# Optimization experiments

Hardware: AMD Instinct MI355X
Metric: run time of the kernel (lower is better)

## Reference

```python
import jax, jax.numpy as jnp
import numpy as np

I, H, NL = 153, 128, 2


def setup_inputs() -> dict:
    key = jax.random.key(0)
    ks = jax.random.split(key, 16)
    s = 1.0 / np.sqrt(H)
    inp = {"x": jax.random.normal(ks[0], (1024, 256, I), dtype=jnp.float32)}
    # GRU layer 0 (input I) and layer 1 (input H), PyTorch layout: W_ih [3H, in], W_hh [3H, H]
    inp["W_ih0"] = jax.random.uniform(ks[1], (3 * H, I), jnp.float32, -s, s)
    inp["W_hh0"] = jax.random.uniform(ks[2], (3 * H, H), jnp.float32, -s, s)
    inp["b_ih0"] = jax.random.uniform(ks[3], (3 * H,), jnp.float32, -s, s)
    inp["b_hh0"] = jax.random.uniform(ks[4], (3 * H,), jnp.float32, -s, s)
    inp["W_ih1"] = jax.random.uniform(ks[5], (3 * H, H), jnp.float32, -s, s)
    inp["W_hh1"] = jax.random.uniform(ks[6], (3 * H, H), jnp.float32, -s, s)
    inp["b_ih1"] = jax.random.uniform(ks[7], (3 * H,), jnp.float32, -s, s)
    inp["b_hh1"] = jax.random.uniform(ks[8], (3 * H,), jnp.float32, -s, s)
    # head: Linear(H,64) -> ReLU -> Linear(64,1) -> Sigmoid (dropout = eval no-op)
    s1 = 1.0 / np.sqrt(H)
    s2 = 1.0 / np.sqrt(64)
    inp["W1"] = jax.random.uniform(ks[9], (64, H), jnp.float32, -s1, s1)
    inp["b1"] = jax.random.uniform(ks[10], (64,), jnp.float32, -s1, s1)
    inp["W2"] = jax.random.uniform(ks[11], (1, 64), jnp.float32, -s2, s2)
    inp["b2"] = jax.random.uniform(ks[12], (1,), jnp.float32, -s2, s2)
    return inp


def _gru_layer(x, W_ih, W_hh, b_ih, b_hh, return_seq):
    # x: [B, T, in]; PyTorch GRU cell equations.
    B, T, _ = x.shape
    gi = jnp.einsum('bti,gi->btg', x, W_ih) + b_ih  # [B, T, 3H] input projection (one big GEMM)
    gi = jnp.transpose(gi, (1, 0, 2))  # [T, B, 3H]
    h0 = jnp.zeros((B, H), dtype=x.dtype)

    def step(h, gi_t):
        gh = h @ W_hh.T + b_hh  # [B, 3H]
        i_r, i_z, i_n = jnp.split(gi_t, 3, axis=-1)
        h_r, h_z, h_n = jnp.split(gh, 3, axis=-1)
        r = jax.nn.sigmoid(i_r + h_r)
        z = jax.nn.sigmoid(i_z + h_z)
        n = jnp.tanh(i_n + r * h_n)
        h_new = (1.0 - z) * n + z * h
        return h_new, (h_new if return_seq else 0.0)

    h_last, ys = jax.lax.scan(step, h0, gi)
    if return_seq:
        return jnp.transpose(ys, (1, 0, 2))  # [B, T, H]
    return h_last  # [B, H]


def reference(x, W_ih0, W_hh0, b_ih0, b_hh0, W_ih1, W_hh1, b_ih1, b_hh1, W1, b1, W2, b2):
    seq0 = _gru_layer(x, W_ih0, W_hh0, b_ih0, b_hh0, return_seq=True)
    last = _gru_layer(seq0, W_ih1, W_hh1, b_ih1, b_hh1, return_seq=False)  # out[:, -1, :]
    hdn = jax.nn.relu(last @ W1.T + b1)
    return jax.nn.sigmoid(hdn @ W2.T + b2)  # [B, 1]
```

## Files before the change

### kernel.cpp

```cpp
#include <hip/hip_runtime.h>


typedef __bf16 bf16x8 __attribute__((ext_vector_type(8)));
typedef __bf16 bf16x4 __attribute__((ext_vector_type(4)));
typedef float  f32x4  __attribute__((ext_vector_type(4)));

#define HS 136
#define OS 136
#define AS 168

__device__ __forceinline__ f32x4 mfma16(bf16x8 a, bf16x8 b, f32x4 c) {
    return __builtin_amdgcn_mfma_f32_16x16x32_bf16(a, b, c, 0, 0, 0);
}
__device__ __forceinline__ float sigf(float x) {
    return __builtin_amdgcn_rcpf(1.f + __expf(-x));
}
__device__ __forceinline__ float tanhf_(float x) { return 2.f * sigf(2.f * x) - 1.f; }

__device__ __forceinline__ void barrier_nodrain() {
    asm volatile("s_waitcnt lgkmcnt(0)" ::: "memory");
    __builtin_amdgcn_s_barrier();
    asm volatile("" ::: "memory");
}

__global__ void prep_w_kernel(const float* __restrict__ Wih0, const float* __restrict__ Whh0,
                              const float* __restrict__ Wih1, const float* __restrict__ Whh1,
                              __bf16* __restrict__ o_ih0, __bf16* __restrict__ o_hh0,
                              __bf16* __restrict__ o_ih1, __bf16* __restrict__ o_hh1) {
    int idx = blockIdx.x * 256 + threadIdx.x;
    if (idx < 384 * 160) {
        int n = idx / 160, k = idx - n * 160;
        o_ih0[idx] = (__bf16)(k < 153 ? Wih0[n * 153 + k] : 0.f);
    }
    if (idx < 384 * 128) {
        o_hh0[idx] = (__bf16)Whh0[idx];
        o_ih1[idx] = (__bf16)Wih1[idx];
        o_hh1[idx] = (__bf16)Whh1[idx];
    }
}

__global__ __launch_bounds__(512, 2) void gi0_gemm_kernel(
    const float* __restrict__ x, const __bf16* __restrict__ Wih0b,
    __bf16* __restrict__ gi0)
{
    __shared__ __align__(16) __bf16 smem[128 * AS];
    const int r0  = blockIdx.x * 128;
    const int tid = threadIdx.x;
    const int w = tid >> 6, lane = tid & 63, q = lane >> 4, c15 = lane & 15;

    bf16x8 bf[3][5];
    #pragma unroll
    for (int j = 0; j < 3; ++j) {
        int colb = 16 * (w + 8 * j) + c15;
        #pragma unroll
        for (int ks = 0; ks < 5; ++ks)
            bf[j][ks] = *(const bf16x8*)(Wih0b + colb * 160 + ks * 32 + q * 8);
    }

    const float* px = x + (size_t)r0 * 153;
    auto scatter = [&](unsigned c, f32x4 v) {
        unsigned m0  = 4u * c;
        unsigned row = m0 / 153u;
        unsigned col = m0 - row * 153u;
        #pragma unroll
        for (int i = 0; i < 4; ++i) {
            unsigned cc = col + i, rr = row;
            if (cc >= 153u) { cc -= 153u; rr += 1u; }
            smem[rr * AS + cc] = (__bf16)v[i];
        }
    };
    #pragma unroll
    for (int p = tid; p < 896; p += 512)
        smem[(p / 7) * AS + 153 + p % 7] = (__bf16)0.f;
    {
        f32x4 v[5];
        #pragma unroll
        for (int k = 0; k < 5; ++k)
            v[k] = *(const f32x4*)(px + 4u * (tid + k * 512));
        #pragma unroll
        for (int k = 0; k < 5; ++k) scatter(tid + k * 512, v[k]);
        f32x4 u[4];
        #pragma unroll
        for (int k = 0; k < 4; ++k)
            u[k] = *(const f32x4*)(px + 4u * (tid + (5 + k) * 512));
        f32x4 tv;
        const bool tail = tid < 288;
        if (tail) tv = *(const f32x4*)(px + 4u * (tid + 4608));
        #pragma unroll
        for (int k = 0; k < 4; ++k) scatter(tid + (5 + k) * 512, u[k]);
        if (tail) scatter(tid + 4608, tv);
    }
    barrier_nodrain();

    f32x4 acc[8][3];
    #pragma unroll
    for (int rt = 0; rt < 8; ++rt)
        #pragma unroll
        for (int j = 0; j < 3; ++j) acc[rt][j] = (f32x4){0.f, 0.f, 0.f, 0.f};

    #pragma unroll
    for (int ks = 0; ks < 5; ++ks) {
        bf16x8 a[8];
        #pragma unroll
        for (int rt = 0; rt < 8; ++rt)
            a[rt] = *(const bf16x8*)(&smem[(rt * 16 + c15) * AS + ks * 32 + q * 8]);
        #pragma unroll
        for (int rt = 0; rt < 8; ++rt)
            #pragma unroll
            for (int j = 0; j < 3; ++j) acc[rt][j] = mfma16(a[rt], bf[j][ks], acc[rt][j]);
    }
    barrier_nodrain();
    #pragma unroll
    for (int j = 0; j < 3; ++j) {
        #pragma unroll
        for (int rt = 0; rt < 8; ++rt)
            #pragma unroll
            for (int r = 0; r < 4; ++r)
                smem[(rt * 16 + q * 4 + r) * OS + 16 * w + c15] = (__bf16)acc[rt][j][r];
        barrier_nodrain();
        #pragma unroll
        for (int pass = 0; pass < 4; ++pass) {
            int row = pass * 32 + (tid >> 4);
            int col = (tid & 15) * 8;
            bf16x8 v = *(const bf16x8*)(&smem[row * OS + col]);
            *(bf16x8*)(gi0 + (size_t)(r0 + row) * 384 + j * 128 + col) = v;
        }
        if (j < 2) barrier_nodrain();
    }
}

__global__ __launch_bounds__(512, 2)
void gru_rec0_kernel(__bf16* __restrict__ gio,
                     const __bf16* __restrict__ Whh0,
                     const float* __restrict__ b_ih0, const float* __restrict__ b_hh0)
{
    __shared__ __align__(16) __bf16 hsA[16 * HS], hsB[16 * HS];

    const int tid  = threadIdx.x;
    const int w    = tid >> 6;
    const int lane = tid & 63;
    const int q    = lane >> 4;
    const int c15  = lane & 15;
    const int c_col = w * 16 + c15;
    const int b0   = blockIdx.x * 16;

    bf16x8 fhh[3][4];
    #pragma unroll
    for (int g = 0; g < 3; ++g)
        #pragma unroll
        for (int ks = 0; ks < 4; ++ks)
            fhh[g][ks] = *(const bf16x8*)(Whh0 + (size_t)(g * 128 + c_col) * 128 + ks * 32 + q * 8);

    float Brz[2], bin, bhn;
    Brz[0] = b_ih0[c_col] + b_hh0[c_col];
    Brz[1] = b_ih0[128 + c_col] + b_hh0[128 + c_col];
    bin = b_ih0[256 + c_col]; bhn = b_hh0[256 + c_col];

    float hr[4] = {0.f, 0.f, 0.f, 0.f};
    for (int i = tid; i < 16 * HS; i += 512) { hsA[i] = (__bf16)0.f; hsB[i] = (__bf16)0.f; }
    __syncthreads();

    unsigned goff[4];
    #pragma unroll
    for (int r = 0; r < 4; ++r)
        goff[r] = (unsigned)(b0 + q * 4 + r) * 98304u + (unsigned)c_col;

    __bf16 gvA[4][3], gvB[4][3];
    #pragma unroll
    for (int r = 0; r < 4; ++r)
        #pragma unroll
        for (int g = 0; g < 3; ++g) gvA[r][g] = gio[goff[r] + g * 128];
    #pragma unroll
    for (int r = 0; r < 4; ++r) goff[r] += 384;

    const int srow = tid >> 5;
    const int scol = (tid & 31) * 4;
    const size_t sbase = (size_t)(b0 + srow) * 98304u + scol;

    auto step = [&](const __bf16* rd, __bf16* wr,
                    __bf16 (&gR)[4][3], __bf16 (&gW)[4][3], int t) {
        #pragma unroll
        for (int r = 0; r < 4; ++r)
            #pragma unroll
            for (int g = 0; g < 3; ++g) gW[r][g] = gio[goff[r] + g * 128];
        #pragma unroll
        for (int r = 0; r < 4; ++r) goff[r] += 384;

        f32x4 hacc[3];
        #pragma unroll
        for (int g = 0; g < 3; ++g) hacc[g] = (f32x4){0.f, 0.f, 0.f, 0.f};
        #pragma unroll
        for (int ks = 0; ks < 4; ++ks) {
            bf16x8 a = *(const bf16x8*)(rd + c15 * HS + ks * 32 + q * 8);
            #pragma unroll
            for (int g = 0; g < 3; ++g) hacc[g] = mfma16(a, fhh[g][ks], hacc[g]);
        }
        #pragma unroll
        for (int r = 0; r < 4; ++r) {
            float rr = sigf((float)gR[r][0] + hacc[0][r] + Brz[0]);
            float zz = sigf((float)gR[r][1] + hacc[1][r] + Brz[1]);
            float nn = tanhf_((float)gR[r][2] + bin + rr * (hacc[2][r] + bhn));
            float hnew = zz * (hr[r] - nn) + nn;
            hr[r] = hnew;
            wr[(q * 4 + r) * HS + c_col] = (__bf16)hnew;
        }
        barrier_nodrain();
        bf16x4 hv = *(const bf16x4*)(wr + srow * HS + scol);
        *(bf16x4*)(gio + sbase + (size_t)t * 384) = hv;
    };

    for (int tt = 0; tt < 128; ++tt) {
        step(hsA, hsB, gvA, gvB, 2 * tt);
        step(hsB, hsA, gvB, gvA, 2 * tt + 1);
    }
}

__global__ __launch_bounds__(512, 2)
void gi1_gemm_kernel(__bf16* __restrict__ gio, const __bf16* __restrict__ Wih1b)
{
    __shared__ __align__(16) __bf16 smem[128 * HS];
    const int r0  = blockIdx.x * 128;
    const int tid = threadIdx.x;
    const int w = tid >> 6, lane = tid & 63, q = lane >> 4, c15 = lane & 15;

    bf16x8 bf[3][4];
    #pragma unroll
    for (int j = 0; j < 3; ++j) {
        int colb = 16 * (w + 8 * j) + c15;
        #pragma unroll
        for (int ks = 0; ks < 4; ++ks)
            bf[j][ks] = *(const bf16x8*)(Wih1b + (size_t)colb * 128 + ks * 32 + q * 8);
    }

    {
        bf16x8 av[4];
        #pragma unroll
        for (int k = 0; k < 4; ++k) {
            int cidx = tid + k * 512;
            int row = cidx >> 4, c8 = (cidx & 15) * 8;
            av[k] = *(const bf16x8*)(gio + (size_t)(r0 + row) * 384 + c8);
        }
        #pragma unroll
        for (int k = 0; k < 4; ++k) {
            int cidx = tid + k * 512;
            int row = cidx >> 4, c8 = (cidx & 15) * 8;
            *(bf16x8*)&smem[row * HS + c8] = av[k];
        }
    }
    barrier_nodrain();

    f32x4 acc[8][3];
    #pragma unroll
    for (int rt = 0; rt < 8; ++rt)
        #pragma unroll
        for (int j = 0; j < 3; ++j) acc[rt][j] = (f32x4){0.f, 0.f, 0.f, 0.f};

    #pragma unroll
    for (int ks = 0; ks < 4; ++ks) {
        bf16x8 a[8];
        #pragma unroll
        for (int rt = 0; rt < 8; ++rt)
            a[rt] = *(const bf16x8*)(&smem[(rt * 16 + c15) * HS + ks * 32 + q * 8]);
        #pragma unroll
        for (int rt = 0; rt < 8; ++rt)
            #pragma unroll
            for (int j = 0; j < 3; ++j) acc[rt][j] = mfma16(a[rt], bf[j][ks], acc[rt][j]);
    }
    barrier_nodrain();
    #pragma unroll
    for (int j = 0; j < 3; ++j) {
        #pragma unroll
        for (int rt = 0; rt < 8; ++rt)
            #pragma unroll
            for (int r = 0; r < 4; ++r)
                smem[(rt * 16 + q * 4 + r) * OS + 16 * w + c15] = (__bf16)acc[rt][j][r];
        barrier_nodrain();
        #pragma unroll
        for (int pass = 0; pass < 4; ++pass) {
            int row = pass * 32 + (tid >> 4);
            int col = (tid & 15) * 8;
            bf16x8 v = *(const bf16x8*)(&smem[row * OS + col]);
            *(bf16x8*)(gio + (size_t)(r0 + row) * 384 + j * 128 + col) = v;
        }
        if (j < 2) barrier_nodrain();
    }
}

__global__ __launch_bounds__(512, 2)
void gru_rec1_kernel(const __bf16* __restrict__ gi1,
                     const __bf16* __restrict__ Whh1,
                     const float* __restrict__ b_ih1, const float* __restrict__ b_hh1,
                     const float* __restrict__ W1, const float* __restrict__ b1,
                     const float* __restrict__ W2, const float* __restrict__ b2,
                     float* __restrict__ out)
{
    __shared__ __align__(16) __bf16 hsA[16 * HS], hsB[16 * HS];
    __shared__ float h1f[16 * 128];
    __shared__ float hdnf[16 * 64];

    const int tid  = threadIdx.x;
    const int w    = tid >> 6;
    const int lane = tid & 63;
    const int q    = lane >> 4;
    const int c15  = lane & 15;
    const int c_col = w * 16 + c15;
    const int b0   = blockIdx.x * 16;

    bf16x8 fhh[3][4];
    #pragma unroll
    for (int g = 0; g < 3; ++g)
        #pragma unroll
        for (int ks = 0; ks < 4; ++ks)
            fhh[g][ks] = *(const bf16x8*)(Whh1 + (size_t)(g * 128 + c_col) * 128 + ks * 32 + q * 8);

    float Brz[2], bin, bhn;
    Brz[0] = b_ih1[c_col] + b_hh1[c_col];
    Brz[1] = b_ih1[128 + c_col] + b_hh1[128 + c_col];
    bin = b_ih1[256 + c_col]; bhn = b_hh1[256 + c_col];

    float hr[4] = {0.f, 0.f, 0.f, 0.f};
    for (int i = tid; i < 16 * HS; i += 512) { hsA[i] = (__bf16)0.f; hsB[i] = (__bf16)0.f; }
    __syncthreads();

    unsigned goff[4];
    #pragma unroll
    for (int r = 0; r < 4; ++r)
        goff[r] = (unsigned)(b0 + q * 4 + r) * 98304u + (unsigned)c_col;

    __bf16 gvA[4][3], gvB[4][3];
    #pragma unroll
    for (int r = 0; r < 4; ++r)
        #pragma unroll
        for (int g = 0; g < 3; ++g) gvA[r][g] = gi1[goff[r] + g * 128];
    #pragma unroll
    for (int r = 0; r < 4; ++r) goff[r] += 384;

    auto step = [&](const __bf16* rd, __bf16* wr,
                    __bf16 (&gR)[4][3], __bf16 (&gW)[4][3]) {
        #pragma unroll
        for (int r = 0; r < 4; ++r)
            #pragma unroll
            for (int g = 0; g < 3; ++g) gW[r][g] = gi1[goff[r] + g * 128];
        #pragma unroll
        for (int r = 0; r < 4; ++r) goff[r] += 384;

        f32x4 hacc[3];
        #pragma unroll
        for (int g = 0; g < 3; ++g) hacc[g] = (f32x4){0.f, 0.f, 0.f, 0.f};
        #pragma unroll
        for (int ks = 0; ks < 4; ++ks) {
            bf16x8 a = *(const bf16x8*)(rd + c15 * HS + ks * 32 + q * 8);
            #pragma unroll
            for (int g = 0; g < 3; ++g) hacc[g] = mfma16(a, fhh[g][ks], hacc[g]);
        }
        #pragma unroll
        for (int r = 0; r < 4; ++r) {
            float rr = sigf((float)gR[r][0] + hacc[0][r] + Brz[0]);
            float zz = sigf((float)gR[r][1] + hacc[1][r] + Brz[1]);
            float nn = tanhf_((float)gR[r][2] + bin + rr * (hacc[2][r] + bhn));
            float hnew = zz * (hr[r] - nn) + nn;
            hr[r] = hnew;
            wr[(q * 4 + r) * HS + c_col] = (__bf16)hnew;
        }
        barrier_nodrain();
    };

    for (int tt = 0; tt < 128; ++tt) {
        step(hsA, hsB, gvA, gvB);
        step(hsB, hsA, gvB, gvA);
    }

    #pragma unroll
    for (int r = 0; r < 4; ++r) h1f[(q * 4 + r) * 128 + c_col] = hr[r];
    __syncthreads();
    for (int p = tid; p < 16 * 64; p += 512) {
        int m = p >> 6, u = p & 63;
        float s = b1[u];
        const float* hrow = &h1f[m * 128];
        const float* wrow = &W1[u * 128];
        #pragma unroll 8
        for (int k = 0; k < 128; ++k) s += hrow[k] * wrow[k];
        hdnf[p] = fmaxf(s, 0.f);
    }
    __syncthreads();
    if (tid < 16) {
        float s = b2[0];
        #pragma unroll 8
        for (int k = 0; k < 64; ++k) s += hdnf[tid * 64 + k] * W2[k];
        out[b0 + tid] = sigf(s);
    }
}

extern "C" void kernel_launch(void* const* d_in, const int* in_sizes, int n_in,
                              void* d_out, int out_size, void* d_ws, size_t ws_size,
                              hipStream_t stream) {
    const float* x     = (const float*)d_in[0];
    const float* W_ih0 = (const float*)d_in[1];
    const float* W_hh0 = (const float*)d_in[2];
    const float* bih0  = (const float*)d_in[3];
    const float* bhh0  = (const float*)d_in[4];
    const float* W_ih1 = (const float*)d_in[5];
    const float* W_hh1 = (const float*)d_in[6];
    const float* bih1  = (const float*)d_in[7];
    const float* bhh1  = (const float*)d_in[8];
    const float* W1    = (const float*)d_in[9];
    const float* b1    = (const float*)d_in[10];
    const float* W2    = (const float*)d_in[11];
    const float* b2    = (const float*)d_in[12];
    float* out = (float*)d_out;

    char* ws = (char*)d_ws;
    __bf16* gio   = (__bf16*)(ws);
    __bf16* wih0b = (__bf16*)(ws + 201326592);
    __bf16* whh0b = (__bf16*)(ws + 201449472);
    __bf16* wih1b = (__bf16*)(ws + 201547776);
    __bf16* whh1b = (__bf16*)(ws + 201646080);

    prep_w_kernel<<<240, 256, 0, stream>>>(W_ih0, W_hh0, W_ih1, W_hh1,
                                           wih0b, whh0b, wih1b, whh1b);
    gi0_gemm_kernel<<<2048, 512, 0, stream>>>(x, wih0b, gio);
    gru_rec0_kernel<<<64, 512, 0, stream>>>(gio, whh0b, bih0, bhh0);
    gi1_gemm_kernel<<<2048, 512, 0, stream>>>(gio, wih1b);
    gru_rec1_kernel<<<64, 512, 0, stream>>>(gio, whh1b, bih1, bhh1,
                                            W1, b1, W2, b2, out);
}
```

Measured before the change: 783.6 us.

## Fuse layer-1 input projection into layer-0 recurrence and store gates time-major

```diff
diff --git a/kernel.cpp b/kernel.cpp
--- a/kernel.cpp
+++ b/kernel.cpp
@@ -2,7 +2,6 @@
 
 
 typedef __bf16 bf16x8 __attribute__((ext_vector_type(8)));
-typedef __bf16 bf16x4 __attribute__((ext_vector_type(4)));
 typedef float  f32x4  __attribute__((ext_vector_type(4)));
 
 #define HS 136
@@ -11,6 +10,10 @@
 
 __device__ __forceinline__ f32x4 mfma16(bf16x8 a, bf16x8 b, f32x4 c) {
     return __builtin_amdgcn_mfma_f32_16x16x32_bf16(a, b, c, 0, 0, 0);
+}
+__device__ __forceinline__ void mfma16_agpr(f32x4& acc, bf16x8 a, const bf16x8& b) {
+    asm("v_mfma_f32_16x16x32_bf16 %0, %1, %2, %0"
+        : "+v"(acc) : "v"(a), "a"(b));
 }
 __device__ __forceinline__ float sigf(float x) {
     return __builtin_amdgcn_rcpf(1.f + __expf(-x));
@@ -47,6 +50,8 @@
     const int r0  = blockIdx.x * 128;
     const int tid = threadIdx.x;
     const int w = tid >> 6, lane = tid & 63, q = lane >> 4, c15 = lane & 15;
+    const int bb = r0 >> 8;
+    const int t0 = r0 & 255;
 
     bf16x8 bf[3][5];
     #pragma unroll
@@ -123,7 +128,8 @@
             int row = pass * 32 + (tid >> 4);
             int col = (tid & 15) * 8;
             bf16x8 v = *(const bf16x8*)(&smem[row * OS + col]);
-            *(bf16x8*)(gi0 + (size_t)(r0 + row) * 384 + j * 128 + col) = v;
+            size_t nrow = (size_t)(t0 + row) * 1024 + bb;
+            *(bf16x8*)(gi0 + nrow * 384 + j * 128 + col) = v;
         }
         if (j < 2) barrier_nodrain();
     }
@@ -132,6 +138,7 @@
 __global__ __launch_bounds__(512, 2)
 void gru_rec0_kernel(__bf16* __restrict__ gio,
                      const __bf16* __restrict__ Whh0,
+                     const __bf16* __restrict__ Wih1b,
                      const float* __restrict__ b_ih0, const float* __restrict__ b_hh0)
 {
     __shared__ __align__(16) __bf16 hsA[16 * HS], hsB[16 * HS];
@@ -144,12 +151,22 @@
     const int c_col = w * 16 + c15;
     const int b0   = blockIdx.x * 16;
 
-    bf16x8 fhh[3][4];
+    bf16x8 fhh[3][4], fih[3][4];
     #pragma unroll
     for (int g = 0; g < 3; ++g)
         #pragma unroll
-        for (int ks = 0; ks < 4; ++ks)
-            fhh[g][ks] = *(const bf16x8*)(Whh0 + (size_t)(g * 128 + c_col) * 128 + ks * 32 + q * 8);
+        for (int ks = 0; ks < 4; ++ks) {
+            size_t off = (size_t)(g * 128 + c_col) * 128 + ks * 32 + q * 8;
+            fhh[g][ks] = *(const bf16x8*)(Whh0 + off);
+            fih[g][ks] = *(const bf16x8*)(Wih1b + off);
+        }
+    #pragma unroll
+    for (int g = 0; g < 3; ++g)
+        #pragma unroll
+        for (int ks = 0; ks < 4; ++ks) {
+            asm volatile("" : "+a"(fhh[g][ks]));
+            asm volatile("" : "+a"(fih[g][ks]));
+        }
 
     float Brz[2], bin, bhn;
     Brz[0] = b_ih0[c_col] + b_hh0[c_col];
@@ -160,40 +177,52 @@
     for (int i = tid; i < 16 * HS; i += 512) { hsA[i] = (__bf16)0.f; hsB[i] = (__bf16)0.f; }
     __syncthreads();
 
-    unsigned goff[4];
+    const size_t TSTRIDE = (size_t)1024 * 384;
+    const __bf16* gp = gio + (size_t)(b0 + q * 4) * 384 + c_col;
+    __bf16*       wp = gio + (size_t)(b0 + q * 4) * 384 + c_col;
+
+    __bf16 gvA[4][3], gvB[4][3];
     #pragma unroll
     for (int r = 0; r < 4; ++r)
-        goff[r] = (unsigned)(b0 + q * 4 + r) * 98304u + (unsigned)c_col;
-
-    __bf16 gvA[4][3], gvB[4][3];
-    #pragma unroll
-    for (int r = 0; r < 4; ++r)
-        #pragma unroll
-        for (int g = 0; g < 3; ++g) gvA[r][g] = gio[goff[r] + g * 128];
-    #pragma unroll
-    for (int r = 0; r < 4; ++r) goff[r] += 384;
-
-    const int srow = tid >> 5;
-    const int scol = (tid & 31) * 4;
-    const size_t sbase = (size_t)(b0 + srow) * 98304u + scol;
-
-    auto step = [&](const __bf16* rd, __bf16* wr,
-                    __bf16 (&gR)[4][3], __bf16 (&gW)[4][3], int t) {
-        #pragma unroll
-        for (int r = 0; r < 4; ++r)
-            #pragma unroll
-            for (int g = 0; g < 3; ++g) gW[r][g] = gio[goff[r] + g * 128];
-        #pragma unroll
-        for (int r = 0; r < 4; ++r) goff[r] += 384;
-
+        #pragma unroll
+        for (int g = 0; g < 3; ++g) gvA[r][g] = gp[r * 384 + g * 128];
+    gp += TSTRIDE;
+
+    auto body = [&](const __bf16* rd, __bf16* wr,
+                    __bf16 (&gR)[4][3], __bf16 (&gW)[4][3],
+                    bool pf, bool st) {
+        if (pf) {
+            #pragma unroll
+            for (int r = 0; r < 4; ++r)
+                #pragma unroll
+                for (int g = 0; g < 3; ++g) gW[r][g] = gp[r * 384 + g * 128];
+            gp += TSTRIDE;
+        }
+        bf16x8 a[4];
+        #pragma unroll
+        for (int ks = 0; ks < 4; ++ks)
+            a[ks] = *(const bf16x8*)(rd + c15 * HS + ks * 32 + q * 8);
         f32x4 hacc[3];
         #pragma unroll
         for (int g = 0; g < 3; ++g) hacc[g] = (f32x4){0.f, 0.f, 0.f, 0.f};
         #pragma unroll
-        for (int ks = 0; ks < 4; ++ks) {
-            bf16x8 a = *(const bf16x8*)(rd + c15 * HS + ks * 32 + q * 8);
-            #pragma unroll
-            for (int g = 0; g < 3; ++g) hacc[g] = mfma16(a, fhh[g][ks], hacc[g]);
+        for (int ks = 0; ks < 4; ++ks)
+            #pragma unroll
+            for (int g = 0; g < 3; ++g) mfma16_agpr(hacc[g], a[ks], fhh[g][ks]);
+        if (st) {
+            f32x4 iacc[3];
+            #pragma unroll
+            for (int g = 0; g < 3; ++g) iacc[g] = (f32x4){0.f, 0.f, 0.f, 0.f};
+            #pragma unroll
+            for (int ks = 0; ks < 4; ++ks)
+                #pragma unroll
+                for (int g = 0; g < 3; ++g) mfma16_agpr(iacc[g], a[ks], fih[g][ks]);
+            #pragma unroll
+            for (int g = 0; g < 3; ++g)
+                #pragma unroll
+                for (int r = 0; r < 4; ++r)
+                    wp[r * 384 + g * 128] = (__bf16)iacc[g][r];
+            wp += TSTRIDE;
         }
         #pragma unroll
         for (int r = 0; r < 4; ++r) {
@@ -205,84 +234,31 @@
             wr[(q * 4 + r) * HS + c_col] = (__bf16)hnew;
         }
         barrier_nodrain();
-        bf16x4 hv = *(const bf16x4*)(wr + srow * HS + scol);
-        *(bf16x4*)(gio + sbase + (size_t)t * 384) = hv;
     };
 
-    for (int tt = 0; tt < 128; ++tt) {
-        step(hsA, hsB, gvA, gvB, 2 * tt);
-        step(hsB, hsA, gvB, gvA, 2 * tt + 1);
-    }
-}
-
-__global__ __launch_bounds__(512, 2)
-void gi1_gemm_kernel(__bf16* __restrict__ gio, const __bf16* __restrict__ Wih1b)
-{
-    __shared__ __align__(16) __bf16 smem[128 * HS];
-    const int r0  = blockIdx.x * 128;
-    const int tid = threadIdx.x;
-    const int w = tid >> 6, lane = tid & 63, q = lane >> 4, c15 = lane & 15;
-
-    bf16x8 bf[3][4];
-    #pragma unroll
-    for (int j = 0; j < 3; ++j) {
-        int colb = 16 * (w + 8 * j) + c15;
-        #pragma unroll
-        for (int ks = 0; ks < 4; ++ks)
-            bf[j][ks] = *(const bf16x8*)(Wih1b + (size_t)colb * 128 + ks * 32 + q * 8);
-    }
-
+    body(hsA, hsB, gvA, gvB, true, false);
+    for (int i = 0; i < 127; ++i) {
+        body(hsB, hsA, gvB, gvA, true, true);
+        body(hsA, hsB, gvA, gvB, true, true);
+    }
+    body(hsB, hsA, gvB, gvA, false, true);
     {
-        bf16x8 av[4];
-        #pragma unroll
-        for (int k = 0; k < 4; ++k) {
-            int cidx = tid + k * 512;
-            int row = cidx >> 4, c8 = (cidx & 15) * 8;
-            av[k] = *(const bf16x8*)(gio + (size_t)(r0 + row) * 384 + c8);
-        }
-        #pragma unroll
-        for (int k = 0; k < 4; ++k) {
-            int cidx = tid + k * 512;
-            int row = cidx >> 4, c8 = (cidx & 15) * 8;
-            *(bf16x8*)&smem[row * HS + c8] = av[k];
-        }
-    }
-    barrier_nodrain();
-
-    f32x4 acc[8][3];
-    #pragma unroll
-    for (int rt = 0; rt < 8; ++rt)
-        #pragma unroll
-        for (int j = 0; j < 3; ++j) acc[rt][j] = (f32x4){0.f, 0.f, 0.f, 0.f};
-
-    #pragma unroll
-    for (int ks = 0; ks < 4; ++ks) {
-        bf16x8 a[8];
-        #pragma unroll
-        for (int rt = 0; rt < 8; ++rt)
-            a[rt] = *(const bf16x8*)(&smem[(rt * 16 + c15) * HS + ks * 32 + q * 8]);
-        #pragma unroll
-        for (int rt = 0; rt < 8; ++rt)
-            #pragma unroll
-            for (int j = 0; j < 3; ++j) acc[rt][j] = mfma16(a[rt], bf[j][ks], acc[rt][j]);
-    }
-    barrier_nodrain();
-    #pragma unroll
-    for (int j = 0; j < 3; ++j) {
-        #pragma unroll
-        for (int rt = 0; rt < 8; ++rt)
+        bf16x8 a[4];
+        #pragma unroll
+        for (int ks = 0; ks < 4; ++ks)
+            a[ks] = *(const bf16x8*)(hsA + c15 * HS + ks * 32 + q * 8);
+        f32x4 iacc[3];
+        #pragma unroll
+        for (int g = 0; g < 3; ++g) iacc[g] = (f32x4){0.f, 0.f, 0.f, 0.f};
+        #pragma unroll
+        for (int ks = 0; ks < 4; ++ks)
+            #pragma unroll
+            for (int g = 0; g < 3; ++g) mfma16_agpr(iacc[g], a[ks], fih[g][ks]);
+        #pragma unroll
+        for (int g = 0; g < 3; ++g)
             #pragma unroll
             for (int r = 0; r < 4; ++r)
-                smem[(rt * 16 + q * 4 + r) * OS + 16 * w + c15] = (__bf16)acc[rt][j][r];
-        barrier_nodrain();
-        #pragma unroll
-        for (int pass = 0; pass < 4; ++pass) {
-            int row = pass * 32 + (tid >> 4);
-            int col = (tid & 15) * 8;
-            bf16x8 v = *(const bf16x8*)(&smem[row * OS + col]);
-            *(bf16x8*)(gio + (size_t)(r0 + row) * 384 + j * 128 + col) = v;
-        }
-        if (j < 2) barrier_nodrain();
+                wp[r * 384 + g * 128] = (__bf16)iacc[g][r];
     }
 }
 
@@ -312,6 +288,11 @@
         #pragma unroll
         for (int ks = 0; ks < 4; ++ks)
             fhh[g][ks] = *(const bf16x8*)(Whh1 + (size_t)(g * 128 + c_col) * 128 + ks * 32 + q * 8);
+    #pragma unroll
+    for (int g = 0; g < 3; ++g)
+        #pragma unroll
+        for (int ks = 0; ks < 4; ++ks)
+            asm volatile("" : "+a"(fhh[g][ks]));
 
     float Brz[2], bin, bhn;
     Brz[0] = b_ih1[c_col] + b_hh1[c_col];
@@ -322,37 +303,36 @@
     for (int i = tid; i < 16 * HS; i += 512) { hsA[i] = (__bf16)0.f; hsB[i] = (__bf16)0.f; }
     __syncthreads();
 
-    unsigned goff[4];
+    const size_t TSTRIDE = (size_t)1024 * 384;
+    const __bf16* gp = gi1 + (size_t)(b0 + q * 4) * 384 + c_col;
+
+    __bf16 gvA[4][3], gvB[4][3];
     #pragma unroll
     for (int r = 0; r < 4; ++r)
-        goff[r] = (unsigned)(b0 + q * 4 + r) * 98304u + (unsigned)c_col;
-
-    __bf16 gvA[4][3], gvB[4][3];
-    #pragma unroll
-    for (int r = 0; r < 4; ++r)
-        #pragma unroll
-        for (int g = 0; g < 3; ++g) gvA[r][g] = gi1[goff[r] + g * 128];
-    #pragma unroll
-    for (int r = 0; r < 4; ++r) goff[r] += 384;
+        #pragma unroll
+        for (int g = 0; g < 3; ++g) gvA[r][g] = gp[r * 384 + g * 128];
+    gp += TSTRIDE;
 
     auto step = [&](const __bf16* rd, __bf16* wr,
-                    __bf16 (&gR)[4][3], __bf16 (&gW)[4][3]) {
-        #pragma unroll
-        for (int r = 0; r < 4; ++r)
-            #pragma unroll
-            for (int g = 0; g < 3; ++g) gW[r][g] = gi1[goff[r] + g * 128];
-        #pragma unroll
-        for (int r = 0; r < 4; ++r) goff[r] += 384;
-
+                    __bf16 (&gR)[4][3], __bf16 (&gW)[4][3], bool pf) {
+        if (pf) {
+            #pragma unroll
+            for (int r = 0; r < 4; ++r)
+                #pragma unroll
+                for (int g = 0; g < 3; ++g) gW[r][g] = gp[r * 384 + g * 128];
+            gp += TSTRIDE;
+        }
+        bf16x8 a[4];
+        #pragma unroll
+        for (int ks = 0; ks < 4; ++ks)
+            a[ks] = *(const bf16x8*)(rd + c15 * HS + ks * 32 + q * 8);
         f32x4 hacc[3];
         #pragma unroll
         for (int g = 0; g < 3; ++g) hacc[g] = (f32x4){0.f, 0.f, 0.f, 0.f};
         #pragma unroll
-        for (int ks = 0; ks < 4; ++ks) {
-            bf16x8 a = *(const bf16x8*)(rd + c15 * HS + ks * 32 + q * 8);
-            #pragma unroll
-            for (int g = 0; g < 3; ++g) hacc[g] = mfma16(a, fhh[g][ks], hacc[g]);
-        }
+        for (int ks = 0; ks < 4; ++ks)
+            #pragma unroll
+            for (int g = 0; g < 3; ++g) mfma16_agpr(hacc[g], a[ks], fhh[g][ks]);
         #pragma unroll
         for (int r = 0; r < 4; ++r) {
             float rr = sigf((float)gR[r][0] + hacc[0][r] + Brz[0]);
@@ -365,9 +345,9 @@
         barrier_nodrain();
     };
 
-    for (int tt = 0; tt < 128; ++tt) {
-        step(hsA, hsB, gvA, gvB);
-        step(hsB, hsA, gvB, gvA);
+    for (int i = 0; i < 128; ++i) {
+        step(hsA, hsB, gvA, gvB, true);
+        step(hsB, hsA, gvB, gvA, i < 127);
     }
 
     #pragma unroll
@@ -419,8 +399,7 @@
     prep_w_kernel<<<240, 256, 0, stream>>>(W_ih0, W_hh0, W_ih1, W_hh1,
                                            wih0b, whh0b, wih1b, whh1b);
     gi0_gemm_kernel<<<2048, 512, 0, stream>>>(x, wih0b, gio);
-    gru_rec0_kernel<<<64, 512, 0, stream>>>(gio, whh0b, bih0, bhh0);
-    gi1_gemm_kernel<<<2048, 512, 0, stream>>>(gio, wih1b);
+    gru_rec0_kernel<<<64, 512, 0, stream>>>(gio, whh0b, wih1b, bih0, bhh0);
     gru_rec1_kernel<<<64, 512, 0, stream>>>(gio, whh1b, bih1, bhh1,
                                             W1, b1, W2, b2, out);
 }
```

Result: slower. 897.6 us (+14.5%).
